# Kernel tuning notes

Hardware: AMD Instinct MI355X
Metric: run time of the kernel (lower is better)

## Reference

```python
import jax, jax.numpy as jnp
import numpy as np

B, N, M, E, H, A = 2048, 768, 8192, 512, 8, 64  # batch, n, m, embed_dim, heads, head_dim(a)


def setup_inputs() -> dict:
    key = jax.random.key(0)
    ks = jax.random.split(key, 16)
    s = 0.02
    return {
        "x": jax.random.normal(ks[0], (B, N), jnp.float32),
        "X_cross": jax.random.normal(ks[1], (M, N), jnp.float32),
        # manual projection weights (used as x @ W, i.e. nn.Linear .weight of shape [out,in] -> here stored [n, E] etc.)
        "W_q_w": jax.random.normal(ks[2], (N, E), jnp.float32) * s,
        "W_k_w": jax.random.normal(ks[3], (N, E), jnp.float32) * s,
        "W_v_w": jax.random.normal(ks[4], (N, N), jnp.float32) * s,
        # nn.MultiheadAttention internal projections (vdim=n -> separate q/k/v weights)
        "q_w": jax.random.normal(ks[5], (E, E), jnp.float32) * s,
        "k_w": jax.random.normal(ks[6], (E, E), jnp.float32) * s,
        "v_w": jax.random.normal(ks[7], (E, N), jnp.float32) * s,
        "b_q": jax.random.normal(ks[8], (E,), jnp.float32) * s,
        "b_k": jax.random.normal(ks[9], (E,), jnp.float32) * s,
        "b_v": jax.random.normal(ks[10], (E,), jnp.float32) * s,
        "out_w": jax.random.normal(ks[11], (E, E), jnp.float32) * s,
        "out_b": jax.random.normal(ks[12], (E,), jnp.float32) * s,
        # final W_o: nn.Linear(E, n)
        "W_o_w": jax.random.normal(ks[13], (N, E), jnp.float32) * s,
        "W_o_b": jax.random.normal(ks[14], (N,), jnp.float32) * s,
    }


def reference(x, X_cross, W_q_w, W_k_w, W_v_w, q_w, k_w, v_w, b_q, b_k, b_v, out_w, out_b, W_o_w, W_o_b):
    inv_sqrt_a = jnp.float32(1.0 / np.sqrt(A))
    # manual projections (note: the F.layer_norm loop in the source is a no-op)
    Q = (x @ W_q_w) * inv_sqrt_a           # [B, E]; extra 1/sqrt(a) scaling applied pre-MHA
    K = X_cross @ W_k_w                    # [m, E]
    V = X_cross @ W_v_w                    # [m, n]
    # nn.MultiheadAttention (unbatched 2D inputs -> seq lens B and m)
    q = (Q @ q_w.T + b_q).reshape(B, H, A)
    k = (K @ k_w.T + b_k).reshape(M, H, A)
    v = (V @ v_w.T + b_v).reshape(M, H, A)
    scores = jnp.einsum('bha,mha->hbm', q, k) * inv_sqrt_a  # MHA's own 1/sqrt(head_dim)
    attn = jax.nn.softmax(scores, axis=-1)                  # [H, B, m]
    f = attn.mean(axis=0)                                   # averaged attn weights [B, m]
    ctx = jnp.einsum('hbm,mha->bha', attn, v).reshape(B, E)
    attn_out = ctx @ out_w.T + out_b                        # MHA out_proj -> [B, E]
    x_hat = attn_out @ W_o_w.T + W_o_b                      # [B, n]
    return (x, x_hat, f, V)
```

## Files before the change

kernel.cpp:

```cpp
#include <hip/hip_runtime.h>
#include <hip/hip_bf16.h>

typedef unsigned short u16;
typedef unsigned int u32;
typedef __attribute__((ext_vector_type(8))) __bf16 bf16x8;
typedef __attribute__((ext_vector_type(4))) float f32x4;

#define Bd  2048
#define Nd  768
#define Md  8192
#define Ed  512
#define Hd  8
#define NSL 8
#define AIT 16

__device__ __forceinline__ u16 f2bf(float f){
    union { __bf16 b; u16 u; } c; c.b = (__bf16)f; return c.u;
}
__device__ __forceinline__ float bf2f(u16 u){
    union { unsigned u; float f; } a; a.u = ((unsigned)u)<<16; return a.f;
}
__device__ __forceinline__ u32 pack2(float a, float b){
    union { ushort2 s; u32 u; } r;
    r.s.x = f2bf(a); r.s.y = f2bf(b);
    return r.u;
}
__device__ __forceinline__ float fexp2(float x){ return __builtin_amdgcn_exp2f(x); }

__device__ __forceinline__ void glds16(const void* g, void* l){
    __builtin_amdgcn_global_load_lds((const __attribute__((address_space(1))) void*)g,
                                     (__attribute__((address_space(3))) void*)l, 16, 0, 0);
}

struct CvtSeg { const float* src; u16* dst; float* dstf; int n4; };
struct Cvt9 { CvtSeg s[9]; };

__global__ void cvt_many_k(Cvt9 a, int total4){
    int i = blockIdx.x*256 + threadIdx.x;
    if (i >= total4) return;
    #pragma unroll
    for (int k=0;k<9;k++){
        if (i < a.s[k].n4){
            float4 v = *(const float4*)(a.s[k].src + (size_t)i*4);
            if (a.s[k].dstf) *(float4*)(a.s[k].dstf + (size_t)i*4) = v;
            ushort4 u; u.x=f2bf(v.x); u.y=f2bf(v.y); u.z=f2bf(v.z); u.w=f2bf(v.w);
            *(ushort4*)(a.s[k].dst + (size_t)i*4) = u;
            return;
        }
        i -= a.s[k].n4;
    }
}

__global__ void tcvt2_k(const float* __restrict__ in0, u16* __restrict__ out0, int R0,
                        const float* __restrict__ in1, u16* __restrict__ out1, int R1){
    __shared__ float t[32][33];
    const float* in; u16* out; int R;
    if (blockIdx.z == 0){ in=in0; out=out0; R=R0; }
    else                { in=in1; out=out1; R=R1; }
    int nb = R/32;
    if ((int)blockIdx.x >= nb || (int)blockIdx.y >= nb) return;
    const int tx = threadIdx.x & 31, ty = threadIdx.x >> 5;
    const int r0 = blockIdx.y*32, c0 = blockIdx.x*32;
    #pragma unroll
    for (int i=0;i<4;i++)
        t[ty + i*8][tx] = in[(size_t)(r0+ty+i*8)*R + c0+tx];
    __syncthreads();
    #pragma unroll
    for (int i=0;i<4;i++)
        out[(size_t)(c0+ty+i*8)*R + r0+tx] = f2bf(t[tx][ty+i*8]);
}

__global__ void gemv_bo_k(const float* __restrict__ W, const float* __restrict__ ob,
                          const float* __restrict__ wob, float* __restrict__ bo){
    const int wave = threadIdx.x >> 6, lane = threadIdx.x & 63;
    const int i = blockIdx.x*4 + wave;
    float s = 0.f;
    for (int j = lane; j < 512; j += 64) s += W[(size_t)i*512 + j] * ob[j];
    #pragma unroll
    for (int off = 32; off; off >>= 1) s += __shfl_down(s, off);
    if (lane == 0) bo[i] = s + wob[i];
}

struct GSeg {
    const u16* A; const u16* B; void* C; const float* bias;
    int M, N, K; float alpha, bscale; int biasmode, outf32, blk0, nbx;
};
struct GBatch { GSeg s[5]; int nseg; };

__global__ __launch_bounds__(256, 2)
void gemm_multi(GBatch gb)
{
    __shared__ u16 lA[128*64];
    __shared__ u16 lB[128*64];
    const int bid = blockIdx.x;
    int si = 0;
    #pragma unroll
    for (int k=1;k<5;k++) if (k < gb.nseg && bid >= gb.s[k].blk0) si = k;
    const GSeg sg = gb.s[si];
    const int local = bid - sg.blk0;
    const int bx = local % sg.nbx, by = local / sg.nbx;
    const int K = sg.K, N = sg.N;

    const int tid = threadIdx.x;
    const int wave = tid >> 6, lane = tid & 63;
    const int wr = wave >> 1, wc = wave & 1;
    const size_t row0 = (size_t)by * 128;
    const size_t col0 = (size_t)bx * 128;

    f32x4 acc[4][4] = {};

    const int srow = wave*32 + (lane>>3);
    const int scol = (lane&7)*8;
    const u16* gA = sg.A + (row0 + srow)*(size_t)K + scol;
    const u16* gB = sg.B + (col0 + srow)*(size_t)K + scol;

    for (int kt = 0; kt < K; kt += 64) {
        #pragma unroll
        for (int i = 0; i < 4; ++i) {
            glds16(gA + (size_t)i*8*K + kt, lA + (wave*32 + i*8)*64);
            glds16(gB + (size_t)i*8*K + kt, lB + (wave*32 + i*8)*64);
        }
        __syncthreads();
        #pragma unroll
        for (int ks = 0; ks < 2; ++ks) {
            bf16x8 af[4], bfv[4];
            #pragma unroll
            for (int i = 0; i < 4; ++i)
                af[i] = *(const bf16x8*)&lA[(wr*64 + i*16 + (lane&15))*64 + ks*32 + (lane>>4)*8];
            #pragma unroll
            for (int i = 0; i < 4; ++i)
                bfv[i] = *(const bf16x8*)&lB[(wc*64 + i*16 + (lane&15))*64 + ks*32 + (lane>>4)*8];
            #pragma unroll
            for (int mi = 0; mi < 4; ++mi)
                #pragma unroll
                for (int ni = 0; ni < 4; ++ni)
                    acc[mi][ni] = __builtin_amdgcn_mfma_f32_16x16x32_bf16(af[mi], bfv[ni], acc[mi][ni], 0, 0, 0);
        }
        __syncthreads();
    }

    #pragma unroll
    for (int mi = 0; mi < 4; ++mi) {
        #pragma unroll
        for (int j = 0; j < 4; ++j) {
            const size_t r = row0 + wr*64 + mi*16 + (lane>>4)*4 + j;
            float badd_r = (sg.biasmode==2) ? sg.bias[r]*sg.bscale : 0.f;
            #pragma unroll
            for (int ni = 0; ni < 4; ++ni) {
                const size_t c = col0 + wc*64 + ni*16 + (lane&15);
                float bv = (sg.biasmode==1) ? sg.bias[c]*sg.bscale : badd_r;
                float v = acc[mi][ni][j] * sg.alpha + bv;
                if (sg.outf32) ((float*)sg.C)[r*(size_t)N + c] = v;
                else           ((u16*)sg.C)[r*(size_t)N + c] = f2bf(v);
            }
        }
    }
}

template<int BIASMODE, int OUTF32>
__global__ __launch_bounds__(256, 2)
void gemm_bt(const u16* __restrict__ A, const u16* __restrict__ B,
             void* __restrict__ C, const float* __restrict__ bias,
             int M, int N, int K, float alpha, float bscale)
{
    __shared__ u16 lA[128*64];
    __shared__ u16 lB[128*64];
    const int tid = threadIdx.x;
    const int wave = tid >> 6, lane = tid & 63;
    const int wr = wave >> 1, wc = wave & 1;
    const size_t row0 = (size_t)blockIdx.y * 128;
    const size_t col0 = (size_t)blockIdx.x * 128;

    f32x4 acc[4][4] = {};

    const int srow = wave*32 + (lane>>3);
    const int scol = (lane&7)*8;
    const u16* gA = A + (row0 + srow)*(size_t)K + scol;
    const u16* gB = B + (col0 + srow)*(size_t)K + scol;

    for (int kt = 0; kt < K; kt += 64) {
        #pragma unroll
        for (int i = 0; i < 4; ++i) {
            glds16(gA + (size_t)i*8*K + kt, lA + (wave*32 + i*8)*64);
            glds16(gB + (size_t)i*8*K + kt, lB + (wave*32 + i*8)*64);
        }
        __syncthreads();
        #pragma unroll
        for (int ks = 0; ks < 2; ++ks) {
            bf16x8 af[4], bfv[4];
            #pragma unroll
            for (int i = 0; i < 4; ++i)
                af[i] = *(const bf16x8*)&lA[(wr*64 + i*16 + (lane&15))*64 + ks*32 + (lane>>4)*8];
            #pragma unroll
            for (int i = 0; i < 4; ++i)
                bfv[i] = *(const bf16x8*)&lB[(wc*64 + i*16 + (lane&15))*64 + ks*32 + (lane>>4)*8];
            #pragma unroll
            for (int mi = 0; mi < 4; ++mi)
                #pragma unroll
                for (int ni = 0; ni < 4; ++ni)
                    acc[mi][ni] = __builtin_amdgcn_mfma_f32_16x16x32_bf16(af[mi], bfv[ni], acc[mi][ni], 0, 0, 0);
        }
        __syncthreads();
    }

    #pragma unroll
    for (int mi = 0; mi < 4; ++mi) {
        #pragma unroll
        for (int j = 0; j < 4; ++j) {
            const size_t r = row0 + wr*64 + mi*16 + (lane>>4)*4 + j;
            float badd_r = (BIASMODE==2) ? bias[r]*bscale : 0.f;
            #pragma unroll
            for (int ni = 0; ni < 4; ++ni) {
                const size_t c = col0 + wc*64 + ni*16 + (lane&15);
                float v = acc[mi][ni][j] * alpha + ((BIASMODE==1) ? bias[c]*bscale : badd_r);
                if (OUTF32) ((float*)C)[r*(size_t)N + c] = v;
                else        ((u16*)C)[r*(size_t)N + c] = f2bf(v);
            }
        }
    }
}

__global__ __launch_bounds__(256, 2)
void attn_sc(const u16* __restrict__ qp, const u16* __restrict__ kp,
             const u16* __restrict__ vTp, float* __restrict__ sumexp,
             u16* __restrict__ part)
{
    __shared__ u16 lK[2][64*64];
    __shared__ u16 lV[2][64*64];
    __shared__ u16 lP[4][64*64];
    const int tid = threadIdx.x, w = tid>>6, l = tid&63;
    const int g = l>>4, b15 = l&15;
    const int h = blockIdx.x & 7;
    const int rest = blockIdx.x >> 3;
    const int msl = rest & (NSL-1), bt = rest >> 3;
    const int m0 = msl * (AIT*64);

    bf16x8 qf[4][2];
    #pragma unroll
    for (int rt=0; rt<4; ++rt)
        #pragma unroll
        for (int ks=0; ks<2; ++ks)
            qf[rt][ks] = *(const bf16x8*)&qp[(size_t)(bt*256 + w*64 + rt*16 + b15)*512
                                            + h*64 + ks*32 + g*8];

    int addrW[4][4], addrR[4][2];
    #pragma unroll
    for (int rt=0; rt<4; ++rt){
        int bl = rt*16 + b15;
        #pragma unroll
        for (int ct=0; ct<4; ++ct){
            int chunk = ct*2 + (g>>1);
            addrW[rt][ct] = bl*128 + ((chunk ^ (bl&7))<<4) + (g&1)*8;
        }
        #pragma unroll
        for (int ks2=0; ks2<2; ++ks2)
            addrR[rt][ks2] = bl*128 + (((ks2*4+g) ^ (bl&7))<<4);
    }

    const int srcc = ((l&7) ^ (l>>3))*8;
    char* lPw = (char*)lP[w];

    auto STAGE = [&](int buf, int mb){
        #pragma unroll
        for (int i=0;i<2;i++)
            glds16(kp + (size_t)(mb + w*16 + i*8 + (l>>3))*512 + h*64 + srcc,
                   &lK[buf][(w*16 + i*8)*64]);
        #pragma unroll
        for (int i=0;i<2;i++)
            glds16(vTp + (size_t)(h*64 + w*16 + i*8 + (l>>3))*8192 + mb + srcc,
                   &lV[buf][(w*16 + i*8)*64]);
    };

    STAGE(0, m0);
    __syncthreads();

    f32x4 cacc[4][4] = {};
    float rs[4] = {};
    int cur = 0;
    for (int t=0; t<AIT; ++t){
        if (t+1 < AIT) STAGE(cur^1, m0 + (t+1)*64);

        f32x4 sacc[4][4] = {};
        #pragma unroll
        for (int ks=0; ks<2; ++ks){
            bf16x8 bk[4];
            #pragma unroll
            for (int ct=0; ct<4; ++ct)
                bk[ct] = *(const bf16x8*)&lK[cur][(ct*16+b15)*64 + (((ks*4+g) ^ (b15&7))<<3)];
            #pragma unroll
            for (int rt=0; rt<4; ++rt)
                #pragma unroll
                for (int ct=0; ct<4; ++ct)
                    sacc[rt][ct] = __builtin_amdgcn_mfma_f32_16x16x32_bf16(bk[ct], qf[rt][ks], sacc[rt][ct],0,0,0);
        }
        #pragma unroll
        for (int rt=0; rt<4; ++rt)
            #pragma unroll
            for (int ct=0; ct<4; ++ct){
                float p0 = fexp2(sacc[rt][ct][0]);
                float p1 = fexp2(sacc[rt][ct][1]);
                float p2 = fexp2(sacc[rt][ct][2]);
                float p3 = fexp2(sacc[rt][ct][3]);
                rs[rt] += (p0+p1)+(p2+p3);
                uint2 pk; pk.x = pack2(p0,p1); pk.y = pack2(p2,p3);
                *(uint2*)(lPw + addrW[rt][ct]) = pk;
            }
        #pragma unroll
        for (int ks2=0; ks2<2; ++ks2){
            bf16x8 vb[4];
            #pragma unroll
            for (int ai=0; ai<4; ++ai)
                vb[ai] = *(const bf16x8*)&lV[cur][(ai*16+b15)*64 + (((ks2*4+g) ^ (b15&7))<<3)];
            #pragma unroll
            for (int rt=0; rt<4; ++rt){
                bf16x8 pa = *(const bf16x8*)(lPw + addrR[rt][ks2]);
                #pragma unroll
                for (int ai=0; ai<4; ++ai)
                    cacc[rt][ai] = __builtin_amdgcn_mfma_f32_16x16x32_bf16(pa, vb[ai], cacc[rt][ai],0,0,0);
            }
        }
        __syncthreads();
        cur ^= 1;
    }

    #pragma unroll
    for (int rt=0; rt<4; ++rt)
        #pragma unroll
        for (int ai=0; ai<4; ++ai)
            #pragma unroll
            for (int j=0; j<4; ++j){
                size_t r = (size_t)bt*256 + w*64 + rt*16 + g*4 + j;
                size_t c = (size_t)h*64 + ai*16 + b15;
                part[((size_t)msl<<20) + r*512 + c] = f2bf(cacc[rt][ai][j]);
            }
    #pragma unroll
    for (int rt=0; rt<4; ++rt){
        float s = rs[rt];
        s += __shfl_xor(s, 16); s += __shfl_xor(s, 32);
        if (l < 16)
            atomicAdd(&sumexp[h*2048 + bt*256 + w*64 + rt*16 + l], s);
    }
}

__global__ __launch_bounds__(256, 3)
void attn_f(const u16* __restrict__ qp, const u16* __restrict__ kp,
            const float* __restrict__ sume, float* __restrict__ fo)
{
    __shared__ u16 lK[2][64*64];
    __shared__ float lR[8*256];
    const int tid = threadIdx.x, w = tid>>6, l = tid&63;
    const int g = l>>4, b15 = l&15;
    const int bid = blockIdx.x;
    const int xcd = bid & 7, r2 = bid >> 3;
    const int mt = xcd*16 + (r2 & 15), bt = r2 >> 4;

    #pragma unroll
    for (int i=0;i<8;i++){
        int id = i*256 + tid;
        lR[id] = 0.125f / sume[(id>>8)*2048 + bt*256 + (id&255)];
    }

    const int srcc = ((l&7) ^ (l>>3))*8;
    auto STAGE = [&](int buf, int h){
        #pragma unroll
        for (int i=0;i<2;i++)
            glds16(kp + (size_t)(mt*64 + w*16 + i*8 + (l>>3))*512 + h*64 + srcc,
                   &lK[buf][(w*16 + i*8)*64]);
    };
    STAGE(0, 0);
    __syncthreads();

    f32x4 facc[4][4] = {};
    int cur = 0;
    for (int h=0; h<8; ++h){
        if (h<7) STAGE(cur^1, h+1);
        bf16x8 qf[4][2];
        #pragma unroll
        for (int rt=0; rt<4; ++rt)
            #pragma unroll
            for (int ks=0; ks<2; ++ks)
                qf[rt][ks] = *(const bf16x8*)&qp[(size_t)(bt*256 + w*64 + rt*16 + b15)*512
                                                + h*64 + ks*32 + g*8];
        #pragma unroll
        for (int ch=0; ch<2; ++ch){
            f32x4 sacc[4][2] = {};
            #pragma unroll
            for (int ks=0; ks<2; ++ks){
                bf16x8 bk[2];
                #pragma unroll
                for (int c2=0; c2<2; ++c2){
                    int ct = ch*2 + c2;
                    bk[c2] = *(const bf16x8*)&lK[cur][(ct*16+b15)*64 + (((ks*4+g) ^ (b15&7))<<3)];
                }
                #pragma unroll
                for (int rt=0; rt<4; ++rt)
                    #pragma unroll
                    for (int c2=0; c2<2; ++c2)
                        sacc[rt][c2] = __builtin_amdgcn_mfma_f32_16x16x32_bf16(bk[c2], qf[rt][ks], sacc[rt][c2],0,0,0);
            }
            #pragma unroll
            for (int rt=0; rt<4; ++rt){
                float ri = lR[h*256 + w*64 + rt*16 + b15];
                #pragma unroll
                for (int c2=0; c2<2; ++c2)
                    #pragma unroll
                    for (int j=0;j<4;j++)
                        facc[rt][ch*2+c2][j] += fexp2(sacc[rt][c2][j]) * ri;
            }
        }
        __syncthreads();
        cur ^= 1;
    }
    #pragma unroll
    for (int rt=0; rt<4; ++rt){
        size_t b = (size_t)bt*256 + w*64 + rt*16 + b15;
        #pragma unroll
        for (int ct=0; ct<4; ++ct)
            *(float4*)&fo[b*8192 + mt*64 + ct*16 + g*4] = *(float4*)&facc[rt][ct];
    }
}

__global__ void ctx_reduce_k(const u16* __restrict__ part, const float* __restrict__ sume,
                             u16* __restrict__ ctx){
    int i = (blockIdx.x*256 + threadIdx.x)*4;
    int b = i >> 9, h = (i >> 6) & 7;
    float ri = 1.0f / sume[h*2048 + b];
    float s0=0.f, s1=0.f, s2=0.f, s3=0.f;
    #pragma unroll
    for (int k=0;k<NSL;k++){
        ushort4 v = *(const ushort4*)(part + ((size_t)k<<20) + i);
        s0 += bf2f(v.x); s1 += bf2f(v.y); s2 += bf2f(v.z); s3 += bf2f(v.w);
    }
    ushort4 u;
    u.x = f2bf(s0*ri); u.y = f2bf(s1*ri); u.z = f2bf(s2*ri); u.w = f2bf(s3*ri);
    *(ushort4*)(ctx + i) = u;
}

extern "C" void kernel_launch(void* const* d_in, const int* in_sizes, int n_in,
                              void* d_out, int out_size, void* d_ws, size_t ws_size,
                              hipStream_t stream)
{
    const float* x   = (const float*)d_in[0];
    const float* Xc  = (const float*)d_in[1];
    const float* Wq  = (const float*)d_in[2];
    const float* Wk  = (const float*)d_in[3];
    const float* Wv  = (const float*)d_in[4];
    const float* qw  = (const float*)d_in[5];
    const float* kw  = (const float*)d_in[6];
    const float* vw  = (const float*)d_in[7];
    const float* bq  = (const float*)d_in[8];
    const float* bk  = (const float*)d_in[9];
    const float* bv  = (const float*)d_in[10];
    const float* ow  = (const float*)d_in[11];
    const float* ob  = (const float*)d_in[12];
    const float* Wo  = (const float*)d_in[13];
    const float* Wob = (const float*)d_in[14];

    float* out_x    = (float*)d_out;
    float* out_xhat = out_x + (size_t)Bd*Nd;
    float* out_f    = out_xhat + (size_t)Bd*Nd;
    float* out_V    = out_f + (size_t)Bd*Md;

    char* wsb = (char*)d_ws;
    size_t off = 0;
    auto alloc = [&](size_t bytes) -> void* {
        void* p = wsb + off; off += (bytes + 255) & ~(size_t)255; return p;
    };
    u16* xb     = (u16*)alloc((size_t)Bd*Nd*2);
    u16* Xb     = (u16*)alloc((size_t)Md*Nd*2);
    u16* qwb    = (u16*)alloc((size_t)Ed*Ed*2);
    u16* kwb    = (u16*)alloc((size_t)Ed*Ed*2);
    u16* vwb    = (u16*)alloc((size_t)Ed*Nd*2);
    u16* Wqb    = (u16*)alloc((size_t)Nd*Ed*2);
    u16* Wkb    = (u16*)alloc((size_t)Nd*Ed*2);
    u16* Wvb    = (u16*)alloc((size_t)Nd*Nd*2);
    u16* WvTb   = (u16*)alloc((size_t)Nd*Nd*2);
    u16* Wo_b   = (u16*)alloc((size_t)Nd*Ed*2);
    u16* owTb   = (u16*)alloc((size_t)Ed*Ed*2);
    u16* WqqT   = (u16*)alloc((size_t)Ed*Nd*2);
    u16* WkkT   = (u16*)alloc((size_t)Ed*Nd*2);
    u16* WvvT   = (u16*)alloc((size_t)Ed*Nd*2);
    u16* Woo2T  = (u16*)alloc((size_t)Nd*Ed*2);
    float* bo   = (float*)alloc((size_t)Nd*4);
    u16* qb     = (u16*)alloc((size_t)Bd*Ed*2);
    u16* kb     = (u16*)alloc((size_t)Md*Ed*2);
    u16* vTb    = (u16*)alloc((size_t)Ed*Md*2);
    u16* ctxb   = (u16*)alloc((size_t)Bd*Ed*2);
    float* sume = (float*)alloc((size_t)Hd*Bd*4);
    u16* part   = (u16*)alloc((size_t)NSL*Bd*Ed*2);
    if (off > ws_size) return;

    hipMemsetAsync(sume, 0, (size_t)Hd*Bd*4, stream);

    const float LOG2E = 1.44269504f;

    Cvt9 ca;
    ca.s[0] = { x,  xb,  out_x, Bd*Nd/4 };
    ca.s[1] = { Xc, Xb,  nullptr, Md*Nd/4 };
    ca.s[2] = { qw, qwb, nullptr, Ed*Ed/4 };
    ca.s[3] = { kw, kwb, nullptr, Ed*Ed/4 };
    ca.s[4] = { vw, vwb, nullptr, Ed*Nd/4 };
    ca.s[5] = { Wq, Wqb, nullptr, Nd*Ed/4 };
    ca.s[6] = { Wk, Wkb, nullptr, Nd*Ed/4 };
    ca.s[7] = { Wv, Wvb, nullptr, Nd*Nd/4 };
    ca.s[8] = { Wo, Wo_b, nullptr, Nd*Ed/4 };
    int total4 = (Bd*Nd + Md*Nd + Ed*Ed*2 + Ed*Nd + Nd*Ed*2 + Nd*Nd + Nd*Ed)/4;
    cvt_many_k<<<(total4+255)/256, 256, 0, stream>>>(ca, total4);
    tcvt2_k<<<dim3(Nd/32, Nd/32, 2), 256, 0, stream>>>(Wv, WvTb, Nd, ow, owTb, Ed);
    gemv_bo_k<<<Nd/4, 256, 0, stream>>>(Wo, ob, Wob, bo);

    {
        GBatch gb; gb.nseg = 5;
        gb.s[0] = { qwb, Wqb, WqqT, nullptr, Ed, Nd, Ed, 0.125f*0.125f*LOG2E, 1.f, 0, 0,   0, Nd/128 };
        gb.s[1] = { kwb, Wkb, WkkT, nullptr, Ed, Nd, Ed, 1.f, 1.f, 0, 0,  24, Nd/128 };
        gb.s[2] = { vwb, Wvb, WvvT, nullptr, Ed, Nd, Nd, 1.f, 1.f, 0, 0,  48, Nd/128 };
        gb.s[3] = { Wo_b, owTb, Woo2T, nullptr, Nd, Ed, Ed, 1.f, 1.f, 0, 0,  72, Ed/128 };
        gb.s[4] = { Xb, WvTb, out_V, nullptr, Md, Nd, Nd, 1.f, 1.f, 0, 1,  96, Nd/128 };
        gemm_multi<<<96 + (Md/128)*(Nd/128), 256, 0, stream>>>(gb);
    }
    {
        GBatch gb; gb.nseg = 3;
        gb.s[0] = { xb, WqqT, qb, bq, Bd, Ed, Nd, 1.f, 0.125f*LOG2E, 1, 0,   0, Ed/128 };
        gb.s[1] = { Xb, WkkT, kb, bk, Md, Ed, Nd, 1.f, 1.f, 1, 0,  64, Ed/128 };
        gb.s[2] = { WvvT, Xb, vTb, bv, Ed, Md, Nd, 1.f, 1.f, 2, 0, 320, Md/128 };
        gb.s[3] = gb.s[0]; gb.s[4] = gb.s[0];
        gemm_multi<<<320 + (Ed/128)*(Md/128), 256, 0, stream>>>(gb);
    }

    attn_sc<<<512, 256, 0, stream>>>(qb, kb, vTb, sume, part);
    attn_f<<<1024, 256, 0, stream>>>(qb, kb, sume, out_f);
    ctx_reduce_k<<<Bd*Ed/1024, 256, 0, stream>>>(part, sume, ctxb);

    gemm_bt<1,1><<<dim3(Nd/128, Bd/128), 256, 0, stream>>>(ctxb, Woo2T, out_xhat, bo, Bd, Nd, Ed, 1.f, 1.f);
}
```

Measured before the change: 197.6 us.

## Merge prep kernels and memset into one launch; fuse attn_f with final GEMM

Folds the fp32-to-bf16 conversion, the two transposes, the bias GEMV and the zeroing of the sum-exp buffer into a single block-dispatched prep kernel. It also merges the averaged-attention kernel and the output projection GEMM into one launch, so the independent GEMM blocks share the machine with the f computation. gemm_multi occupancy hint goes from 2 to 3 blocks per CU. The aim is fewer launches and less tail idle time, at the cost of heterogeneous blocks and possible register pressure from the higher occupancy bound.

```diff
diff --git a/kernel.cpp b/kernel.cpp
--- a/kernel.cpp
+++ b/kernel.cpp
@@ -33,52 +33,71 @@
 }
 
 struct CvtSeg { const float* src; u16* dst; float* dstf; int n4; };
-struct Cvt9 { CvtSeg s[9]; };
-
-__global__ void cvt_many_k(Cvt9 a, int total4){
-    int i = blockIdx.x*256 + threadIdx.x;
-    if (i >= total4) return;
-    #pragma unroll
-    for (int k=0;k<9;k++){
-        if (i < a.s[k].n4){
-            float4 v = *(const float4*)(a.s[k].src + (size_t)i*4);
-            if (a.s[k].dstf) *(float4*)(a.s[k].dstf + (size_t)i*4) = v;
-            ushort4 u; u.x=f2bf(v.x); u.y=f2bf(v.y); u.z=f2bf(v.z); u.w=f2bf(v.w);
-            *(ushort4*)(a.s[k].dst + (size_t)i*4) = u;
-            return;
-        }
-        i -= a.s[k].n4;
-    }
-}
-
-__global__ void tcvt2_k(const float* __restrict__ in0, u16* __restrict__ out0, int R0,
-                        const float* __restrict__ in1, u16* __restrict__ out1, int R1){
+struct PrepArgs {
+    CvtSeg s[9]; int total4;
+    const float* Wv; u16* WvT;
+    const float* ow; u16* owT;
+    const float* Wo; const float* ob; const float* Wob; float* bo;
+    float* sume;
+};
+#define PREP_CVT_BLKS 10320
+#define TCVT0_BLKS 576
+#define TCVT1_BLKS 256
+#define GEMV_BLKS 192
+#define ZERO_BLKS 16
+
+__global__ __launch_bounds__(256, 8)
+void prep_k(PrepArgs a){
     __shared__ float t[32][33];
-    const float* in; u16* out; int R;
-    if (blockIdx.z == 0){ in=in0; out=out0; R=R0; }
-    else                { in=in1; out=out1; R=R1; }
-    int nb = R/32;
-    if ((int)blockIdx.x >= nb || (int)blockIdx.y >= nb) return;
-    const int tx = threadIdx.x & 31, ty = threadIdx.x >> 5;
-    const int r0 = blockIdx.y*32, c0 = blockIdx.x*32;
-    #pragma unroll
-    for (int i=0;i<4;i++)
-        t[ty + i*8][tx] = in[(size_t)(r0+ty+i*8)*R + c0+tx];
-    __syncthreads();
-    #pragma unroll
-    for (int i=0;i<4;i++)
-        out[(size_t)(c0+ty+i*8)*R + r0+tx] = f2bf(t[tx][ty+i*8]);
-}
-
-__global__ void gemv_bo_k(const float* __restrict__ W, const float* __restrict__ ob,
-                          const float* __restrict__ wob, float* __restrict__ bo){
-    const int wave = threadIdx.x >> 6, lane = threadIdx.x & 63;
-    const int i = blockIdx.x*4 + wave;
-    float s = 0.f;
-    for (int j = lane; j < 512; j += 64) s += W[(size_t)i*512 + j] * ob[j];
-    #pragma unroll
-    for (int off = 32; off; off >>= 1) s += __shfl_down(s, off);
-    if (lane == 0) bo[i] = s + wob[i];
+    const int bid = blockIdx.x, tid = threadIdx.x;
+    if (bid < PREP_CVT_BLKS){
+        int i = bid*256 + tid;
+        if (i >= a.total4) return;
+        #pragma unroll
+        for (int k=0;k<9;k++){
+            if (i < a.s[k].n4){
+                float4 v = *(const float4*)(a.s[k].src + (size_t)i*4);
+                if (a.s[k].dstf) *(float4*)(a.s[k].dstf + (size_t)i*4) = v;
+                ushort4 u; u.x=f2bf(v.x); u.y=f2bf(v.y); u.z=f2bf(v.z); u.w=f2bf(v.w);
+                *(ushort4*)(a.s[k].dst + (size_t)i*4) = u;
+                return;
+            }
+            i -= a.s[k].n4;
+        }
+        return;
+    }
+    int local = bid - PREP_CVT_BLKS;
+    if (local < TCVT0_BLKS + TCVT1_BLKS){
+        const float* in; u16* out; int R, bx, by;
+        if (local < TCVT0_BLKS){ in=a.Wv; out=a.WvT; R=Nd; bx=local%24; by=local/24; }
+        else { int l2=local-TCVT0_BLKS; in=a.ow; out=a.owT; R=Ed; bx=l2%16; by=l2/16; }
+        const int tx = tid & 31, ty = tid >> 5;
+        const int r0 = by*32, c0 = bx*32;
+        #pragma unroll
+        for (int i=0;i<4;i++)
+            t[ty + i*8][tx] = in[(size_t)(r0+ty+i*8)*R + c0+tx];
+        __syncthreads();
+        #pragma unroll
+        for (int i=0;i<4;i++)
+            out[(size_t)(c0+ty+i*8)*R + r0+tx] = f2bf(t[tx][ty+i*8]);
+        return;
+    }
+    local -= TCVT0_BLKS + TCVT1_BLKS;
+    if (local < GEMV_BLKS){
+        const int wave = tid >> 6, lane = tid & 63;
+        const int i = local*4 + wave;
+        float s = 0.f;
+        for (int j = lane; j < 512; j += 64) s += a.Wo[(size_t)i*512 + j] * a.ob[j];
+        #pragma unroll
+        for (int off = 32; off; off >>= 1) s += __shfl_down(s, off);
+        if (lane == 0) a.bo[i] = s + a.Wob[i];
+        return;
+    }
+    local -= GEMV_BLKS;
+    {
+        int idx = local*1024 + tid*4;
+        *(float4*)(a.sume + idx) = make_float4(0.f,0.f,0.f,0.f);
+    }
 }
 
 struct GSeg {
@@ -87,7 +106,7 @@
 };
 struct GBatch { GSeg s[5]; int nseg; };
 
-__global__ __launch_bounds__(256, 2)
+__global__ __launch_bounds__(256, 3)
 void gemm_multi(GBatch gb)
 {
     __shared__ u16 lA[128*64];
@@ -152,69 +171,6 @@
                 float v = acc[mi][ni][j] * sg.alpha + bv;
                 if (sg.outf32) ((float*)sg.C)[r*(size_t)N + c] = v;
                 else           ((u16*)sg.C)[r*(size_t)N + c] = f2bf(v);
-            }
-        }
-    }
-}
-
-template<int BIASMODE, int OUTF32>
-__global__ __launch_bounds__(256, 2)
-void gemm_bt(const u16* __restrict__ A, const u16* __restrict__ B,
-             void* __restrict__ C, const float* __restrict__ bias,
-             int M, int N, int K, float alpha, float bscale)
-{
-    __shared__ u16 lA[128*64];
-    __shared__ u16 lB[128*64];
-    const int tid = threadIdx.x;
-    const int wave = tid >> 6, lane = tid & 63;
-    const int wr = wave >> 1, wc = wave & 1;
-    const size_t row0 = (size_t)blockIdx.y * 128;
-    const size_t col0 = (size_t)blockIdx.x * 128;
-
-    f32x4 acc[4][4] = {};
-
-    const int srow = wave*32 + (lane>>3);
-    const int scol = (lane&7)*8;
-    const u16* gA = A + (row0 + srow)*(size_t)K + scol;
-    const u16* gB = B + (col0 + srow)*(size_t)K + scol;
-
-    for (int kt = 0; kt < K; kt += 64) {
-        #pragma unroll
-        for (int i = 0; i < 4; ++i) {
-            glds16(gA + (size_t)i*8*K + kt, lA + (wave*32 + i*8)*64);
-            glds16(gB + (size_t)i*8*K + kt, lB + (wave*32 + i*8)*64);
-        }
-        __syncthreads();
-        #pragma unroll
-        for (int ks = 0; ks < 2; ++ks) {
-            bf16x8 af[4], bfv[4];
-            #pragma unroll
-            for (int i = 0; i < 4; ++i)
-                af[i] = *(const bf16x8*)&lA[(wr*64 + i*16 + (lane&15))*64 + ks*32 + (lane>>4)*8];
-            #pragma unroll
-            for (int i = 0; i < 4; ++i)
-                bfv[i] = *(const bf16x8*)&lB[(wc*64 + i*16 + (lane&15))*64 + ks*32 + (lane>>4)*8];
-            #pragma unroll
-            for (int mi = 0; mi < 4; ++mi)
-                #pragma unroll
-                for (int ni = 0; ni < 4; ++ni)
-                    acc[mi][ni] = __builtin_amdgcn_mfma_f32_16x16x32_bf16(af[mi], bfv[ni], acc[mi][ni], 0, 0, 0);
-        }
-        __syncthreads();
-    }
-
-    #pragma unroll
-    for (int mi = 0; mi < 4; ++mi) {
-        #pragma unroll
-        for (int j = 0; j < 4; ++j) {
-            const size_t r = row0 + wr*64 + mi*16 + (lane>>4)*4 + j;
-            float badd_r = (BIASMODE==2) ? bias[r]*bscale : 0.f;
-            #pragma unroll
-            for (int ni = 0; ni < 4; ++ni) {
-                const size_t c = col0 + wc*64 + ni*16 + (lane&15);
-                float v = acc[mi][ni][j] * alpha + ((BIASMODE==1) ? bias[c]*bscale : badd_r);
-                if (OUTF32) ((float*)C)[r*(size_t)N + c] = v;
-                else        ((u16*)C)[r*(size_t)N + c] = f2bf(v);
             }
         }
     }
@@ -342,84 +298,6 @@
     }
 }
 
-__global__ __launch_bounds__(256, 3)
-void attn_f(const u16* __restrict__ qp, const u16* __restrict__ kp,
-            const float* __restrict__ sume, float* __restrict__ fo)
-{
-    __shared__ u16 lK[2][64*64];
-    __shared__ float lR[8*256];
-    const int tid = threadIdx.x, w = tid>>6, l = tid&63;
-    const int g = l>>4, b15 = l&15;
-    const int bid = blockIdx.x;
-    const int xcd = bid & 7, r2 = bid >> 3;
-    const int mt = xcd*16 + (r2 & 15), bt = r2 >> 4;
-
-    #pragma unroll
-    for (int i=0;i<8;i++){
-        int id = i*256 + tid;
-        lR[id] = 0.125f / sume[(id>>8)*2048 + bt*256 + (id&255)];
-    }
-
-    const int srcc = ((l&7) ^ (l>>3))*8;
-    auto STAGE = [&](int buf, int h){
-        #pragma unroll
-        for (int i=0;i<2;i++)
-            glds16(kp + (size_t)(mt*64 + w*16 + i*8 + (l>>3))*512 + h*64 + srcc,
-                   &lK[buf][(w*16 + i*8)*64]);
-    };
-    STAGE(0, 0);
-    __syncthreads();
-
-    f32x4 facc[4][4] = {};
-    int cur = 0;
-    for (int h=0; h<8; ++h){
-        if (h<7) STAGE(cur^1, h+1);
-        bf16x8 qf[4][2];
-        #pragma unroll
-        for (int rt=0; rt<4; ++rt)
-            #pragma unroll
-            for (int ks=0; ks<2; ++ks)
-                qf[rt][ks] = *(const bf16x8*)&qp[(size_t)(bt*256 + w*64 + rt*16 + b15)*512
-                                                + h*64 + ks*32 + g*8];
-        #pragma unroll
-        for (int ch=0; ch<2; ++ch){
-            f32x4 sacc[4][2] = {};
-            #pragma unroll
-            for (int ks=0; ks<2; ++ks){
-                bf16x8 bk[2];
-                #pragma unroll
-                for (int c2=0; c2<2; ++c2){
-                    int ct = ch*2 + c2;
-                    bk[c2] = *(const bf16x8*)&lK[cur][(ct*16+b15)*64 + (((ks*4+g) ^ (b15&7))<<3)];
-                }
-                #pragma unroll
-                for (int rt=0; rt<4; ++rt)
-                    #pragma unroll
-                    for (int c2=0; c2<2; ++c2)
-                        sacc[rt][c2] = __builtin_amdgcn_mfma_f32_16x16x32_bf16(bk[c2], qf[rt][ks], sacc[rt][c2],0,0,0);
-            }
-            #pragma unroll
-            for (int rt=0; rt<4; ++rt){
-                float ri = lR[h*256 + w*64 + rt*16 + b15];
-                #pragma unroll
-                for (int c2=0; c2<2; ++c2)
-                    #pragma unroll
-                    for (int j=0;j<4;j++)
-                        facc[rt][ch*2+c2][j] += fexp2(sacc[rt][c2][j]) * ri;
-            }
-        }
-        __syncthreads();
-        cur ^= 1;
-    }
-    #pragma unroll
-    for (int rt=0; rt<4; ++rt){
-        size_t b = (size_t)bt*256 + w*64 + rt*16 + b15;
-        #pragma unroll
-        for (int ct=0; ct<4; ++ct)
-            *(float4*)&fo[b*8192 + mt*64 + ct*16 + g*4] = *(float4*)&facc[rt][ct];
-    }
-}
-
 __global__ void ctx_reduce_k(const u16* __restrict__ part, const float* __restrict__ sume,
                              u16* __restrict__ ctx){
     int i = (blockIdx.x*256 + threadIdx.x)*4;
@@ -434,6 +312,145 @@
     ushort4 u;
     u.x = f2bf(s0*ri); u.y = f2bf(s1*ri); u.z = f2bf(s2*ri); u.w = f2bf(s3*ri);
     *(ushort4*)(ctx + i) = u;
+}
+
+struct FinArgs {
+    const u16* ctxb; const u16* Woo2T; const float* bo; float* out_xhat;
+    const u16* qp; const u16* kp; const float* sume; float* fo;
+};
+#define EPB 96
+
+__global__ __launch_bounds__(256, 3)
+void fin_k(FinArgs fa)
+{
+    __shared__ char smem[32768];
+    const int tid = threadIdx.x;
+
+    if (blockIdx.x < EPB){
+        u16* lA = (u16*)smem;
+        u16* lB = (u16*)(smem + 16384);
+        const int local = blockIdx.x;
+        const int bx = local % 6, by = local / 6;
+        const int K = Ed, N = Nd;
+        const int wave = tid >> 6, lane = tid & 63;
+        const int wr = wave >> 1, wc = wave & 1;
+        const size_t row0 = (size_t)by * 128;
+        const size_t col0 = (size_t)bx * 128;
+        f32x4 acc[4][4] = {};
+        const int srow = wave*32 + (lane>>3);
+        const int scol = (lane&7)*8;
+        const u16* gA = fa.ctxb + (row0 + srow)*(size_t)K + scol;
+        const u16* gB = fa.Woo2T + (col0 + srow)*(size_t)K + scol;
+        for (int kt = 0; kt < K; kt += 64) {
+            #pragma unroll
+            for (int i = 0; i < 4; ++i) {
+                glds16(gA + (size_t)i*8*K + kt, lA + (wave*32 + i*8)*64);
+                glds16(gB + (size_t)i*8*K + kt, lB + (wave*32 + i*8)*64);
+            }
+            __syncthreads();
+            #pragma unroll
+            for (int ks = 0; ks < 2; ++ks) {
+                bf16x8 af[4], bfv[4];
+                #pragma unroll
+                for (int i = 0; i < 4; ++i)
+                    af[i] = *(const bf16x8*)&lA[(wr*64 + i*16 + (lane&15))*64 + ks*32 + (lane>>4)*8];
+                #pragma unroll
+                for (int i = 0; i < 4; ++i)
+                    bfv[i] = *(const bf16x8*)&lB[(wc*64 + i*16 + (lane&15))*64 + ks*32 + (lane>>4)*8];
+                #pragma unroll
+                for (int mi = 0; mi < 4; ++mi)
+                    #pragma unroll
+                    for (int ni = 0; ni < 4; ++ni)
+                        acc[mi][ni] = __builtin_amdgcn_mfma_f32_16x16x32_bf16(af[mi], bfv[ni], acc[mi][ni], 0, 0, 0);
+            }
+            __syncthreads();
+        }
+        #pragma unroll
+        for (int mi = 0; mi < 4; ++mi)
+            #pragma unroll
+            for (int j = 0; j < 4; ++j) {
+                const size_t r = row0 + wr*64 + mi*16 + (lane>>4)*4 + j;
+                #pragma unroll
+                for (int ni = 0; ni < 4; ++ni) {
+                    const size_t c = col0 + wc*64 + ni*16 + (lane&15);
+                    fa.out_xhat[r*(size_t)N + c] = acc[mi][ni][j] + fa.bo[c];
+                }
+            }
+        return;
+    }
+
+    u16* lK0 = (u16*)smem;
+    float* lR = (float*)(smem + 16384);
+    const int w = tid>>6, l = tid&63;
+    const int g = l>>4, b15 = l&15;
+    const int bid = blockIdx.x - EPB;
+    const int xcd = bid & 7, r2 = bid >> 3;
+    const int mt = xcd*16 + (r2 & 15), bt = r2 >> 4;
+
+    #pragma unroll
+    for (int i=0;i<8;i++){
+        int id = i*256 + tid;
+        lR[id] = 0.125f / fa.sume[(id>>8)*2048 + bt*256 + (id&255)];
+    }
+
+    const int srcc = ((l&7) ^ (l>>3))*8;
+    auto STAGE = [&](int buf, int h){
+        #pragma unroll
+        for (int i=0;i<2;i++)
+            glds16(fa.kp + (size_t)(mt*64 + w*16 + i*8 + (l>>3))*512 + h*64 + srcc,
+                   lK0 + buf*4096 + (w*16 + i*8)*64);
+    };
+    STAGE(0, 0);
+    __syncthreads();
+
+    f32x4 facc[4][4] = {};
+    int cur = 0;
+    for (int h=0; h<8; ++h){
+        if (h<7) STAGE(cur^1, h+1);
+        bf16x8 qf[4][2];
+        #pragma unroll
+        for (int rt=0; rt<4; ++rt)
+            #pragma unroll
+            for (int ks=0; ks<2; ++ks)
+                qf[rt][ks] = *(const bf16x8*)&fa.qp[(size_t)(bt*256 + w*64 + rt*16 + b15)*512
+                                                    + h*64 + ks*32 + g*8];
+        #pragma unroll
+        for (int ch=0; ch<2; ++ch){
+            f32x4 sacc[4][2] = {};
+            #pragma unroll
+            for (int ks=0; ks<2; ++ks){
+                bf16x8 bk[2];
+                #pragma unroll
+                for (int c2=0; c2<2; ++c2){
+                    int ct = ch*2 + c2;
+                    bk[c2] = *(const bf16x8*)&lK0[cur*4096 + (ct*16+b15)*64 + (((ks*4+g) ^ (b15&7))<<3)];
+                }
+                #pragma unroll
+                for (int rt=0; rt<4; ++rt)
+                    #pragma unroll
+                    for (int c2=0; c2<2; ++c2)
+                        sacc[rt][c2] = __builtin_amdgcn_mfma_f32_16x16x32_bf16(bk[c2], qf[rt][ks], sacc[rt][c2],0,0,0);
+            }
+            #pragma unroll
+            for (int rt=0; rt<4; ++rt){
+                float ri = lR[h*256 + w*64 + rt*16 + b15];
+                #pragma unroll
+                for (int c2=0; c2<2; ++c2)
+                    #pragma unroll
+                    for (int j=0;j<4;j++)
+                        facc[rt][ch*2+c2][j] += fexp2(sacc[rt][c2][j]) * ri;
+            }
+        }
+        __syncthreads();
+        cur ^= 1;
+    }
+    #pragma unroll
+    for (int rt=0; rt<4; ++rt){
+        size_t b = (size_t)bt*256 + w*64 + rt*16 + b15;
+        #pragma unroll
+        for (int ct=0; ct<4; ++ct)
+            *(float4*)&fa.fo[b*8192 + mt*64 + ct*16 + g*4] = *(float4*)&facc[rt][ct];
+    }
 }
 
 extern "C" void kernel_launch(void* const* d_in, const int* in_sizes, int n_in,
@@ -490,24 +507,23 @@
     u16* part   = (u16*)alloc((size_t)NSL*Bd*Ed*2);
     if (off > ws_size) return;
 
-    hipMemsetAsync(sume, 0, (size_t)Hd*Bd*4, stream);
-
     const float LOG2E = 1.44269504f;
 
-    Cvt9 ca;
-    ca.s[0] = { x,  xb,  out_x, Bd*Nd/4 };
-    ca.s[1] = { Xc, Xb,  nullptr, Md*Nd/4 };
-    ca.s[2] = { qw, qwb, nullptr, Ed*Ed/4 };
-    ca.s[3] = { kw, kwb, nullptr, Ed*Ed/4 };
-    ca.s[4] = { vw, vwb, nullptr, Ed*Nd/4 };
-    ca.s[5] = { Wq, Wqb, nullptr, Nd*Ed/4 };
-    ca.s[6] = { Wk, Wkb, nullptr, Nd*Ed/4 };
-    ca.s[7] = { Wv, Wvb, nullptr, Nd*Nd/4 };
-    ca.s[8] = { Wo, Wo_b, nullptr, Nd*Ed/4 };
-    int total4 = (Bd*Nd + Md*Nd + Ed*Ed*2 + Ed*Nd + Nd*Ed*2 + Nd*Nd + Nd*Ed)/4;
-    cvt_many_k<<<(total4+255)/256, 256, 0, stream>>>(ca, total4);
-    tcvt2_k<<<dim3(Nd/32, Nd/32, 2), 256, 0, stream>>>(Wv, WvTb, Nd, ow, owTb, Ed);
-    gemv_bo_k<<<Nd/4, 256, 0, stream>>>(Wo, ob, Wob, bo);
+    PrepArgs pa;
+    pa.s[0] = { x,  xb,  out_x,   Bd*Nd/4 };
+    pa.s[1] = { Xc, Xb,  nullptr, Md*Nd/4 };
+    pa.s[2] = { qw, qwb, nullptr, Ed*Ed/4 };
+    pa.s[3] = { kw, kwb, nullptr, Ed*Ed/4 };
+    pa.s[4] = { vw, vwb, nullptr, Ed*Nd/4 };
+    pa.s[5] = { Wq, Wqb, nullptr, Nd*Ed/4 };
+    pa.s[6] = { Wk, Wkb, nullptr, Nd*Ed/4 };
+    pa.s[7] = { Wv, Wvb, nullptr, Nd*Nd/4 };
+    pa.s[8] = { Wo, Wo_b, nullptr, Nd*Ed/4 };
+    pa.total4 = (Bd*Nd + Md*Nd + Ed*Ed*2 + Ed*Nd + Nd*Ed*2 + Nd*Nd + Nd*Ed)/4;
+    pa.Wv = Wv; pa.WvT = WvTb; pa.ow = ow; pa.owT = owTb;
+    pa.Wo = Wo; pa.ob = ob; pa.Wob = Wob; pa.bo = bo;
+    pa.sume = sume;
+    prep_k<<<PREP_CVT_BLKS + TCVT0_BLKS + TCVT1_BLKS + GEMV_BLKS + ZERO_BLKS, 256, 0, stream>>>(pa);
 
     {
         GBatch gb; gb.nseg = 5;
@@ -528,8 +544,7 @@
     }
 
     attn_sc<<<512, 256, 0, stream>>>(qb, kb, vTb, sume, part);
-    attn_f<<<1024, 256, 0, stream>>>(qb, kb, sume, out_f);
     ctx_reduce_k<<<Bd*Ed/1024, 256, 0, stream>>>(part, sume, ctxb);
-
-    gemm_bt<1,1><<<dim3(Nd/128, Bd/128), 256, 0, stream>>>(ctxb, Woo2T, out_xhat, bo, Bd, Nd, Ed, 1.f, 1.f);
-}
+    FinArgs fa = { ctxb, Woo2T, bo, out_xhat, qb, kb, sume, out_f };
+    fin_k<<<EPB + 1024, 256, 0, stream>>>(fa);
+}
```

Result: faster. 179.2 us, median of 2 (-9.3%).
